# Kernel tuning notes

Measured on AMD Instinct MI355X. Metric: run time of the kernel, lower is better.

Reference implementation:

```python
import jax, jax.numpy as jnp
import numpy as np

B, S, I, H, O = 8, 2048, 1024, 4096, 1024


def setup_inputs() -> dict:
    key = jax.random.key(0)
    ks = jax.random.split(key, 7)
    s_i = 1.0 / np.sqrt(I)
    s_h = 1.0 / np.sqrt(H)
    return {
        "x": jax.random.normal(ks[0], (B, S, I), dtype=jnp.float32),
        "W1": jax.random.normal(ks[1], (H, I), dtype=jnp.float32) * s_i,
        "b1": jax.random.normal(ks[2], (H,), dtype=jnp.float32) * s_i,
        "W2": jax.random.normal(ks[3], (O, H), dtype=jnp.float32) * s_h,
        "b2": jax.random.normal(ks[4], (O,), dtype=jnp.float32) * s_h,
        "Wg": jax.random.normal(ks[5], (I, I), dtype=jnp.float32) * s_i,
        "bg": jax.random.normal(ks[6], (I,), dtype=jnp.float32) * s_i,
    }


def reference(x, W1, b1, W2, b2, Wg, bg):
    # Gate is a per-timestep linear on x_t only -> batch it over all timesteps.
    decay = jax.nn.sigmoid(jnp.einsum('bsi,ji->bsj', x, Wg) + bg)  # [B,S,I]
    immediate = x * decay
    delayed = (1.0 - decay) * x

    # Sequential buffer recurrence: buf_t = buf_{t-1} * decay_t + delayed_t
    def step(buf, td):
        d, dl = td
        buf = buf * d + dl
        return buf, buf

    buf0 = jnp.zeros((x.shape[0], x.shape[2]), dtype=x.dtype)
    _, bufs = jax.lax.scan(step, buf0, (jnp.swapaxes(decay, 0, 1), jnp.swapaxes(delayed, 0, 1)))  # [S,B,I]
    combined = immediate + jnp.swapaxes(bufs, 0, 1)  # [B,S,I]

    # MLP applied per timestep -> batch over (B,S).
    hidden = jax.nn.relu(jnp.einsum('bsi,hi->bsh', combined, W1) + b1)  # [B,S,H]
    out = jnp.einsum('bsh,oh->bso', hidden, W2) + b2  # [B,S,O]
    return out
```

## Files before the change

kernel.cpp:

```cpp
#include <hip/hip_runtime.h>
#include <hip/hip_bf16.h>
#include <type_traits>

using bf16 = __hip_bfloat16;

typedef __bf16 bf16x8 __attribute__((ext_vector_type(8)));
typedef unsigned short u16x8 __attribute__((ext_vector_type(8)));
typedef float f32x4 __attribute__((ext_vector_type(4)));

constexpr int Bdim = 8, Sdim = 2048, Idim = 1024, Hdim = 4096, Odim = 1024;
constexpr int CH = 64;
constexpr int CL = Sdim / CH;

#define EP_SIGMOID 0
#define EP_RELU    1
#define EP_BIAS    2

__device__ __forceinline__ void async16(void* lds, const void* g) {
    __builtin_amdgcn_global_load_lds(
        (const __attribute__((address_space(1))) unsigned int*)g,
        (__attribute__((address_space(3))) unsigned int*)lds,
        16, 0, 0);
}

__global__ __launch_bounds__(256) void cvt_f32_bf16(const float* __restrict__ in,
                                                    bf16* __restrict__ out, int n) {
    const int i = (blockIdx.x * 256 + threadIdx.x) * 4;
    if (i >= n) return;
    const float4 v = *(const float4*)(in + i);
    union { unsigned short us[4]; unsigned long long u64; } r;
    r.us[0] = __bfloat16_as_ushort(__float2bfloat16(v.x));
    r.us[1] = __bfloat16_as_ushort(__float2bfloat16(v.y));
    r.us[2] = __bfloat16_as_ushort(__float2bfloat16(v.z));
    r.us[3] = __bfloat16_as_ushort(__float2bfloat16(v.w));
    *(unsigned long long*)(out + i) = r.u64;
}

__device__ __forceinline__ u16x8 load8(const float* p) {
    const float4 v0 = *(const float4*)p;
    const float4 v1 = *(const float4*)(p + 4);
    u16x8 r;
    r[0] = __bfloat16_as_ushort(__float2bfloat16(v0.x));
    r[1] = __bfloat16_as_ushort(__float2bfloat16(v0.y));
    r[2] = __bfloat16_as_ushort(__float2bfloat16(v0.z));
    r[3] = __bfloat16_as_ushort(__float2bfloat16(v0.w));
    r[4] = __bfloat16_as_ushort(__float2bfloat16(v1.x));
    r[5] = __bfloat16_as_ushort(__float2bfloat16(v1.y));
    r[6] = __bfloat16_as_ushort(__float2bfloat16(v1.z));
    r[7] = __bfloat16_as_ushort(__float2bfloat16(v1.w));
    return r;
}
__device__ __forceinline__ u16x8 load8(const bf16* p) { return *(const u16x8*)p; }

__device__ __forceinline__ float toF(float v) { return v; }
__device__ __forceinline__ float toF(bf16 v)  { return __bfloat162float(v); }

__device__ __forceinline__ void ld4(const bf16* p, float f[4]) {
    const ushort4 v = *(const ushort4*)p;
    f[0] = __bfloat162float(__builtin_bit_cast(bf16, v.x));
    f[1] = __bfloat162float(__builtin_bit_cast(bf16, v.y));
    f[2] = __bfloat162float(__builtin_bit_cast(bf16, v.z));
    f[3] = __bfloat162float(__builtin_bit_cast(bf16, v.w));
}
__device__ __forceinline__ void ld4(const float* p, float f[4]) {
    const float4 v = *(const float4*)p;
    f[0] = v.x; f[1] = v.y; f[2] = v.z; f[3] = v.w;
}

template <int MODE, int N, int K, typename TA, typename TB, typename TO>
__global__ __launch_bounds__(256) void gemm_bt(const TA* __restrict__ A,
                                               const TB* __restrict__ Bm,
                                               const float* __restrict__ bias,
                                               TO* __restrict__ outp,
                                               int Mt) {
    __shared__ __align__(16) unsigned short Alds[128 * 32];
    __shared__ __align__(16) unsigned short Blds[128 * 32];

    const int tid  = threadIdx.x;
    const int lane = tid & 63;
    const int wave = tid >> 6;
    const int wr = wave >> 1, wc = wave & 1;
    const int quad = lane >> 4, l15 = lane & 15;

    constexpr int Nt = N >> 7;
    constexpr int GRP = 8;
    constexpr int gsz = GRP * Nt;
    const int g   = blockIdx.x / gsz;
    const int rem = blockIdx.x - g * gsz;
    const int mbase = g * GRP;
    int msz = Mt - mbase; if (msz > GRP) msz = GRP;
    const int m_idx = mbase + rem % msz;
    const int n_idx = rem / msz;
    const int m0 = m_idx * 128;
    const int n0 = n_idx * 128;

    const int srow = tid >> 2;
    const int scol = (tid & 3) * 8;
    const TA* ag0 = A  + (size_t)(m0 + srow) * K + scol;
    const TA* ag1 = ag0 + (size_t)64 * K;
    const TB* bg0 = Bm + (size_t)(n0 + srow) * K + scol;
    const TB* bg1 = bg0 + (size_t)64 * K;
    unsigned short* al0 = Alds + tid * 8;
    unsigned short* al1 = al0 + 2048;
    unsigned short* bl0 = Blds + tid * 8;
    unsigned short* bl1 = bl0 + 2048;

    f32x4 acc[4][4];
#pragma unroll
    for (int i = 0; i < 4; ++i)
#pragma unroll
        for (int j = 0; j < 4; ++j) acc[i][j] = {0.f, 0.f, 0.f, 0.f};

    constexpr bool FAST = std::is_same_v<TA, bf16> && std::is_same_v<TB, bf16>;

#pragma unroll 8
    for (int k0 = 0; k0 < K; k0 += 32) {
        if constexpr (FAST) {
            async16(al0, ag0); async16(al1, ag1);
            async16(bl0, bg0); async16(bl1, bg1);
        } else {
            const u16x8 a0 = load8(ag0), a1 = load8(ag1);
            const u16x8 b0 = load8(bg0), b1 = load8(bg1);
            *(u16x8*)al0 = a0; *(u16x8*)al1 = a1;
            *(u16x8*)bl0 = b0; *(u16x8*)bl1 = b1;
        }
        ag0 += 32; ag1 += 32; bg0 += 32; bg1 += 32;
        __syncthreads();

        bf16x8 af[4], bfv[4];
#pragma unroll
        for (int mi = 0; mi < 4; ++mi) {
            const u16x8 t = *(const u16x8*)(Alds + (wr * 64 + mi * 16 + l15) * 32 + quad * 8);
            af[mi] = __builtin_bit_cast(bf16x8, t);
        }
#pragma unroll
        for (int ni = 0; ni < 4; ++ni) {
            const u16x8 t = *(const u16x8*)(Blds + (wc * 64 + ni * 16 + l15) * 32 + quad * 8);
            bfv[ni] = __builtin_bit_cast(bf16x8, t);
        }
#pragma unroll
        for (int mi = 0; mi < 4; ++mi)
#pragma unroll
            for (int ni = 0; ni < 4; ++ni)
                acc[mi][ni] = __builtin_amdgcn_mfma_f32_16x16x32_bf16(af[mi], bfv[ni], acc[mi][ni], 0, 0, 0);
        __syncthreads();
    }

#pragma unroll
    for (int ni = 0; ni < 4; ++ni) {
        const int ncol = n0 + wc * 64 + ni * 16 + l15;
        const float bv = bias[ncol];
#pragma unroll
        for (int mi = 0; mi < 4; ++mi) {
            const int mrow = m0 + wr * 64 + mi * 16 + quad * 4;
#pragma unroll
            for (int r = 0; r < 4; ++r) {
                float v = acc[mi][ni][r] + bv;
                if constexpr (MODE == EP_SIGMOID) v = 1.f / (1.f + __expf(-v));
                if constexpr (MODE == EP_RELU)    v = v > 0.f ? v : 0.f;
                if constexpr (std::is_same_v<TO, bf16>)
                    outp[(size_t)(mrow + r) * N + ncol] = __float2bfloat16(v);
                else
                    outp[(size_t)(mrow + r) * N + ncol] = v;
            }
        }
    }
}

template <int MODE, int BM, int N, int K, typename TO>
__global__ __launch_bounds__(512, 2) void gemm8p(const bf16* __restrict__ A,
                                                 const bf16* __restrict__ Bm,
                                                 const float* __restrict__ bias,
                                                 TO* __restrict__ outp,
                                                 int Mt) {
    static_assert(BM == 256 || BM == 128);
    constexpr int MR   = BM / 32;
    constexpr int MR2  = MR / 2;
    constexpr int ABUF = BM * 128;
    constexpr int BBUF = 256 * 128;
    constexpr int HALF_A = ABUF / 2;
    constexpr int HALF_B = BBUF / 2;
    constexpr int LA = BM / 128;
    constexpr int NT = K / 64;
    static_assert(NT % 2 == 0 && NT >= 2);

    __shared__ __align__(16) char lds[2 * ABUF + 2 * BBUF];

    const int tid  = threadIdx.x;
    const int lane = tid & 63;
    const int wave = tid >> 6;
    const int wr = wave >> 2;
    const int wc = wave & 3;
    const int quad = lane >> 4, l15 = lane & 15;

    constexpr int Nt = N / 256;
    const int nwg = Mt * Nt;
    int b = blockIdx.x;
    if ((nwg & 7) == 0) { const int cpx = nwg >> 3; b = (b & 7) * cpx + (b >> 3); }
    const int m_idx = b % Mt;
    const int n_idx = b / Mt;
    const int m0 = m_idx * BM;
    const int n0 = n_idx * 256;

    const int loff = (l15 * 64 + quad * 16) ^ ((l15 >> 3) << 5);

    char* const Ab0 = lds;
    char* const Ab1 = lds + ABUF;
    char* const Bb0 = lds + 2 * ABUF;
    char* const Bb1 = lds + 2 * ABUF + BBUF;

    int rowS[2], klS[2];
#pragma unroll
    for (int l = 0; l < 2; ++l) {
        const int s = l * 512 + tid;
        const int c = s & 63;
        const int e = c ^ (((c >> 5) & 1) << 1);
        rowS[l] = ((s >> 7) << 4) + (e >> 2);
        klS[l]  = ((s >> 6) & 1) * 32 + (e & 3) * 8;
    }
    const bf16* pa[2]; const bf16* pb[2];
#pragma unroll
    for (int l = 0; l < 2; ++l) {
        pa[l] = A  + (size_t)(m0 + rowS[l]) * K + klS[l];
        pb[l] = Bm + (size_t)(n0 + rowS[l]) * K + klS[l];
    }

    auto stageA = [&](char* dst, int h, int kt) {
#pragma unroll
        for (int l = 0; l < LA; ++l)
            async16(dst + h * HALF_A + (l * 512 + tid) * 16,
                    pa[l] + (size_t)h * (BM / 2) * K + (size_t)kt * 64);
    };
    auto stageB = [&](char* dst, int h, int kt) {
#pragma unroll
        for (int l = 0; l < 2; ++l)
            async16(dst + h * HALF_B + (l * 512 + tid) * 16,
                    pb[l] + (size_t)h * 128 * K + (size_t)kt * 64);
    };
    auto ldA = [&](const char* abase, int mi_g, int ks) -> bf16x8 {
        return __builtin_bit_cast(bf16x8,
            *(const u16x8*)(abase + (((wr * MR + mi_g) * 2 + ks) << 10) + loff));
    };
    auto ldB = [&](const char* bbase, int ni, int ks) -> bf16x8 {
        return __builtin_bit_cast(bf16x8,
            *(const u16x8*)(bbase + (((wc * 4 + ni) * 2 + ks) << 10) + loff));
    };

    f32x4 acc[MR][4];
#pragma unroll
    for (int i = 0; i < MR; ++i)
#pragma unroll
        for (int j = 0; j < 4; ++j) acc[i][j] = {0.f, 0.f, 0.f, 0.f};
    bf16x8 a[MR2][2], bb[4][2];

    stageA(Ab0, 0, 0); stageA(Ab0, 1, 0);
    stageB(Bb0, 0, 0); stageB(Bb0, 1, 0);
    stageB(Bb1, 0, 1); stageB(Bb1, 1, 1);
    asm volatile("s_waitcnt vmcnt(4)" ::: "memory");
    __builtin_amdgcn_s_barrier();

#define FENCE() asm volatile("" ::: "memory")
#define MFMA_Q(AR, NI0)                                                         \
    _Pragma("unroll") for (int mi = 0; mi < MR2; ++mi)                          \
    _Pragma("unroll") for (int ni = 0; ni < 2; ++ni)                            \
    _Pragma("unroll") for (int ks = 0; ks < 2; ++ks)                            \
        acc[(AR) + mi][(NI0) + ni] = __builtin_amdgcn_mfma_f32_16x16x32_bf16(   \
            a[mi][ks], bb[(NI0) + ni][ks], acc[(AR) + mi][(NI0) + ni], 0, 0, 0);

#define KTILE(T, AB, BB, AN)                                                    \
    {                                                                           \
        const int t_ = (T);                                                     \
                                     \
        _Pragma("unroll") for (int mi = 0; mi < MR2; ++mi)                      \
        _Pragma("unroll") for (int ks = 0; ks < 2; ++ks)                        \
            a[mi][ks] = ldA(AB, mi, ks);                                        \
        _Pragma("unroll") for (int ni = 0; ni < 2; ++ni)                        \
        _Pragma("unroll") for (int ks = 0; ks < 2; ++ks)                        \
            bb[ni][ks] = ldB(BB, ni, ks);                                       \
        if (t_ + 1 < NT) stageA(AN, 0, t_ + 1);                                 \
        FENCE(); __builtin_amdgcn_s_barrier(); FENCE();                         \
        __builtin_amdgcn_s_setprio(1);                                          \
        MFMA_Q(0, 0)                                                            \
        __builtin_amdgcn_s_setprio(0);                                          \
                                            \
        _Pragma("unroll") for (int ni = 0; ni < 2; ++ni)                        \
        _Pragma("unroll") for (int ks = 0; ks < 2; ++ks)                        \
            bb[2 + ni][ks] = ldB(BB, 2 + ni, ks);                               \
        if (t_ + 1 < NT) stageA(AN, 1, t_ + 1);                                 \
        FENCE(); __builtin_amdgcn_s_barrier(); FENCE();                         \
        __builtin_amdgcn_s_setprio(1);                                          \
        MFMA_Q(0, 2)                                                            \
        __builtin_amdgcn_s_setprio(0);                                          \
                                                           \
        _Pragma("unroll") for (int mi = 0; mi < MR2; ++mi)                      \
        _Pragma("unroll") for (int ks = 0; ks < 2; ++ks)                        \
            a[mi][ks] = ldA(AB, MR2 + mi, ks);                                  \
        FENCE(); __builtin_amdgcn_s_barrier(); FENCE();                         \
        __builtin_amdgcn_s_setprio(1);                                          \
        MFMA_Q(MR2, 0)                                                          \
        __builtin_amdgcn_s_setprio(0);                                          \
                       \
        if (t_ + 2 < NT) { stageB(BB, 0, t_ + 2); stageB(BB, 1, t_ + 2); }      \
        if (t_ + 2 < NT) { asm volatile("s_waitcnt vmcnt(4)" ::: "memory"); }   \
        else             { asm volatile("s_waitcnt vmcnt(0)" ::: "memory"); }   \
        FENCE(); __builtin_amdgcn_s_barrier(); FENCE();                         \
        __builtin_amdgcn_s_setprio(1);                                          \
        MFMA_Q(MR2, 2)                                                          \
        __builtin_amdgcn_s_setprio(0);                                          \
    }

#pragma unroll 1
    for (int t = 0; t < NT; t += 2) {
        KTILE(t,     Ab0, Bb0, Ab1)
        KTILE(t + 1, Ab1, Bb1, Ab0)
    }
#undef KTILE
#undef MFMA_Q
#undef FENCE

    float bv[4];
#pragma unroll
    for (int ni = 0; ni < 4; ++ni) bv[ni] = bias[n0 + wc * 64 + ni * 16 + l15];
#pragma unroll
    for (int mi = 0; mi < MR; ++mi) {
        const int mrow = m0 + wr * (MR * 16) + mi * 16 + quad * 4;
#pragma unroll
        for (int r = 0; r < 4; ++r) {
            TO* rowp = outp + (size_t)(mrow + r) * N + n0 + wc * 64 + l15;
#pragma unroll
            for (int ni = 0; ni < 4; ++ni) {
                float v = acc[mi][ni][r] + bv[ni];
                if constexpr (MODE == EP_SIGMOID) v = 1.f / (1.f + __expf(-v));
                if constexpr (MODE == EP_RELU)    v = v > 0.f ? v : 0.f;
                if constexpr (std::is_same_v<TO, bf16>)
                    rowp[ni * 16] = __float2bfloat16(v);
                else
                    rowp[ni * 16] = v;
            }
        }
    }
}

template <typename XT>
__global__ __launch_bounds__(256) void scan_p1(const XT* __restrict__ x,
                                               const bf16* __restrict__ decay,
                                               float* __restrict__ P,
                                               float* __restrict__ Q) {
    const int bc = blockIdx.x;
    const int c = bc & (CH - 1);
    const int b = bc / CH;
    const int i = threadIdx.x * 4;
    size_t idx = ((size_t)(b * Sdim + c * CL)) * Idim + i;
    float p[4] = {1.f, 1.f, 1.f, 1.f};
    float q[4] = {0.f, 0.f, 0.f, 0.f};
#pragma unroll 4
    for (int j = 0; j < CL; ++j) {
        float d[4], xx[4];
        ld4(decay + idx, d);
        ld4(x + idx, xx);
#pragma unroll
        for (int k = 0; k < 4; ++k) {
            q[k] = q[k] * d[k] + (1.f - d[k]) * xx[k];
            p[k] *= d[k];
        }
        idx += Idim;
    }
    *(float4*)(P + (size_t)bc * Idim + i) = {p[0], p[1], p[2], p[3]};
    *(float4*)(Q + (size_t)bc * Idim + i) = {q[0], q[1], q[2], q[3]};
}

__global__ __launch_bounds__(256) void scan_p2(const float* __restrict__ P,
                                               const float* __restrict__ Q,
                                               float* __restrict__ buf0,
                                               int G) {
    const int g = blockIdx.x * 256 + threadIdx.x;
    const int b = g >> 10;
    const int i = g & (Idim - 1);
    if (b >= G) return;
    float buf = 0.f;
    for (int c = 0; c < CH; ++c) {
        const size_t o = ((size_t)(b * CH + c)) * Idim + i;
        buf0[o] = buf;
        buf = P[o] * buf + Q[o];
    }
}

template <typename XT>
__global__ __launch_bounds__(256) void scan_p3(const XT* __restrict__ x,
                                               const bf16* __restrict__ decay,
                                               const float* __restrict__ buf0,
                                               bf16* __restrict__ comb) {
    const int bc = blockIdx.x;
    const int c = bc & (CH - 1);
    const int b = bc / CH;
    const int i = threadIdx.x * 4;
    size_t idx = ((size_t)(b * Sdim + c * CL)) * Idim + i;
    float buf[4];
    {
        const float4 v = *(const float4*)(buf0 + (size_t)bc * Idim + i);
        buf[0] = v.x; buf[1] = v.y; buf[2] = v.z; buf[3] = v.w;
    }
#pragma unroll 4
    for (int j = 0; j < CL; ++j) {
        float d[4], xx[4];
        ld4(decay + idx, d);
        ld4(x + idx, xx);
        ushort4 o;
#pragma unroll
        for (int k = 0; k < 4; ++k)
            buf[k] = buf[k] * d[k] + (1.f - d[k]) * xx[k];
        o.x = __bfloat16_as_ushort(__float2bfloat16(xx[0] * d[0] + buf[0]));
        o.y = __bfloat16_as_ushort(__float2bfloat16(xx[1] * d[1] + buf[1]));
        o.z = __bfloat16_as_ushort(__float2bfloat16(xx[2] * d[2] + buf[2]));
        o.w = __bfloat16_as_ushort(__float2bfloat16(xx[3] * d[3] + buf[3]));
        *(ushort4*)(comb + idx) = o;
        idx += Idim;
    }
}

extern "C" void kernel_launch(void* const* d_in, const int* in_sizes, int n_in,
                              void* d_out, int out_size, void* d_ws, size_t ws_size,
                              hipStream_t stream) {
    const float* x  = (const float*)d_in[0];
    const float* W1 = (const float*)d_in[1];
    const float* b1 = (const float*)d_in[2];
    const float* W2 = (const float*)d_in[3];
    const float* b2 = (const float*)d_in[4];
    const float* Wg = (const float*)d_in[5];
    const float* bg = (const float*)d_in[6];
    float* out = (float*)d_out;

    const dim3 blk(256);
    const dim3 blk512(512);

    const size_t nW1 = (size_t)Hdim * Idim;
    const size_t nW2 = (size_t)Odim * Hdim;
    const size_t nWg = (size_t)Idim * Idim;
    const size_t wCopies = (nW1 + nW2 + nWg) * 2;

    const size_t xbB   = (size_t)Sdim * Idim * 2;
    const size_t dB    = xbB;
    const size_t cmbB  = xbB;
    const size_t pB    = (size_t)CH * Idim * 4;
    const size_t perBatch = xbB + dB + cmbB + 3 * pB;

    int G = 0;
    if (ws_size >= wCopies + 8 * perBatch) G = 8;
    else if (ws_size >= wCopies + 4 * perBatch) G = 4;
    else if (ws_size >= wCopies + 2 * perBatch) G = 2;
    else if (ws_size >= wCopies + 1 * perBatch) G = 1;

    if (G > 0) {
        char* p = (char*)d_ws;
        bf16* W1b = (bf16*)p;  p += nW1 * 2;
        bf16* W2b = (bf16*)p;  p += nW2 * 2;
        bf16* Wgb = (bf16*)p;  p += nWg * 2;
        bf16*  xb   = (bf16*)p;
        bf16*  decay= (bf16*)(p + (size_t)G * xbB);
        bf16*  comb = (bf16*)(p + (size_t)G * (xbB + dB));
        float* P    = (float*)(p + (size_t)G * (xbB + dB + cmbB));
        float* Q    = (float*)(p + (size_t)G * (xbB + dB + cmbB + pB));
        float* buf0 = (float*)(p + (size_t)G * (xbB + dB + cmbB + 2 * pB));
        bf16*  hid  = xb;
        const int chunk_rows = G * 1024;

        cvt_f32_bf16<<<(int)(nW1 / 1024), blk, 0, stream>>>(W1, W1b, (int)nW1);
        cvt_f32_bf16<<<(int)(nW2 / 1024), blk, 0, stream>>>(W2, W2b, (int)nW2);
        cvt_f32_bf16<<<(int)(nWg / 1024), blk, 0, stream>>>(Wg, Wgb, (int)nWg);

        for (int b0 = 0; b0 < Bdim; b0 += G) {
            const float* xg = x + (size_t)b0 * Sdim * Idim;
            const int rowsG = G * Sdim;
            const int nXg = rowsG * Idim;

            cvt_f32_bf16<<<nXg / 1024, blk, 0, stream>>>(xg, xb, nXg);

            gemm8p<EP_SIGMOID, 256, Idim, Idim, bf16>
                <<<(rowsG / 256) * (Idim / 256), blk512, 0, stream>>>(
                    xb, Wgb, bg, decay, rowsG / 256);

            scan_p1<bf16><<<G * CH, blk, 0, stream>>>(xb, decay, P, Q);
            scan_p2<<<G * Idim / 256, blk, 0, stream>>>(P, Q, buf0, G);
            scan_p3<bf16><<<G * CH, blk, 0, stream>>>(xb, decay, buf0, comb);

            for (int r0 = 0; r0 < rowsG; r0 += chunk_rows) {
                const int rows = (rowsG - r0 < chunk_rows) ? rowsG - r0 : chunk_rows;
                gemm8p<EP_RELU, 256, Hdim, Idim, bf16>
                    <<<(rows / 256) * (Hdim / 256), blk512, 0, stream>>>(
                        comb + (size_t)r0 * Idim, W1b, b1, hid, rows / 256);
                gemm8p<EP_BIAS, 128, Odim, Hdim, float>
                    <<<(rows / 128) * (Odim / 256), blk512, 0, stream>>>(
                        hid, W2b, b2, out + (size_t)(b0 * Sdim + r0) * Odim, rows / 128);
            }
        }
    } else {
        char* p = (char*)d_ws;
        bf16*  decay= (bf16*)p;
        bf16*  comb = (bf16*)(p + dB);
        float* P    = (float*)(p + dB + cmbB);
        float* Q    = (float*)(p + dB + cmbB + pB);
        float* buf0 = (float*)(p + dB + cmbB + 2 * pB);
        char*  hp   = p + dB + cmbB + 3 * pB;
        size_t rem  = (ws_size > (size_t)(hp - (char*)d_ws))
                        ? ws_size - (size_t)(hp - (char*)d_ws) : 0;
        int chunk_rows = (int)((rem / ((size_t)Hdim * 2)) / 128) * 128;
        if (chunk_rows < 128) chunk_rows = 128;
        if (chunk_rows > Sdim) chunk_rows = Sdim;
        bf16* hid = (bf16*)hp;

        for (int b0 = 0; b0 < Bdim; ++b0) {
            const float* xg = x + (size_t)b0 * Sdim * Idim;

            gemm_bt<EP_SIGMOID, Idim, Idim, float, float, bf16>
                <<<(Idim / 128) * (Sdim / 128), blk, 0, stream>>>(
                    xg, Wg, bg, decay, Sdim / 128);

            scan_p1<float><<<CH, blk, 0, stream>>>(xg, decay, P, Q);
            scan_p2<<<Idim / 256, blk, 0, stream>>>(P, Q, buf0, 1);
            scan_p3<float><<<CH, blk, 0, stream>>>(xg, decay, buf0, comb);

            for (int r0 = 0; r0 < Sdim; r0 += chunk_rows) {
                const int rows = (Sdim - r0 < chunk_rows) ? Sdim - r0 : chunk_rows;
                gemm_bt<EP_RELU, Hdim, Idim, bf16, float, bf16>
                    <<<(Hdim / 128) * (rows / 128), blk, 0, stream>>>(
                        comb + (size_t)r0 * Idim, W1, b1, hid, rows / 128);
                gemm_bt<EP_BIAS, Odim, Hdim, bf16, float, float>
                    <<<(Odim / 128) * (rows / 128), blk, 0, stream>>>(
                        hid, W2, b2, out + (size_t)(b0 * Sdim + r0) * Odim, rows / 128);
            }
        }
    }
}
```

Baseline: 504.3 us.

## Restructure GEMM main loop to prefetch next-tile fragments and cut barriers

Reorganizes the k-tile loop of the bf16 MFMA GEMM to use four distinct fragment register sets (aL, aH, b0f, b2f). The first A and B fragments of the next tile are loaded from LDS during the last MFMA quarter of the current tile, and barriers per tile drop from four to two. This aims to overlap LDS reads with matrix math and reduce synchronization stalls, at the cost of more VGPRs per thread. The scan chunk length CH also doubles from 64 to 128, changing the chunked recurrence granularity.

```diff
diff --git a/kernel.cpp b/kernel.cpp
--- a/kernel.cpp
+++ b/kernel.cpp
@@ -9,7 +9,7 @@
 typedef float f32x4 __attribute__((ext_vector_type(4)));
 
 constexpr int Bdim = 8, Sdim = 2048, Idim = 1024, Hdim = 4096, Odim = 1024;
-constexpr int CH = 64;
+constexpr int CH = 128;
 constexpr int CL = Sdim / CH;
 
 #define EP_SIGMOID 0
@@ -182,7 +182,7 @@
     constexpr int HALF_B = BBUF / 2;
     constexpr int LA = BM / 128;
     constexpr int NT = K / 64;
-    static_assert(NT % 2 == 0 && NT >= 2);
+    static_assert(NT % 2 == 0 && NT >= 4);
 
     __shared__ __align__(16) char lds[2 * ABUF + 2 * BBUF];
 
@@ -203,6 +203,8 @@
     const int n0 = n_idx * 256;
 
     const int loff = (l15 * 64 + quad * 16) ^ ((l15 >> 3) << 5);
+    const int aol = wr * (MR * 2048) + loff;
+    const int bol = wc * 8192 + loff;
 
     char* const Ab0 = lds;
     char* const Ab1 = lds + ABUF;
@@ -239,11 +241,11 @@
     };
     auto ldA = [&](const char* abase, int mi_g, int ks) -> bf16x8 {
         return __builtin_bit_cast(bf16x8,
-            *(const u16x8*)(abase + (((wr * MR + mi_g) * 2 + ks) << 10) + loff));
+            *(const u16x8*)(abase + aol + (((mi_g) * 2 + ks) << 10)));
     };
     auto ldB = [&](const char* bbase, int ni, int ks) -> bf16x8 {
         return __builtin_bit_cast(bf16x8,
-            *(const u16x8*)(bbase + (((wc * 4 + ni) * 2 + ks) << 10) + loff));
+            *(const u16x8*)(bbase + bol + (((ni) * 2 + ks) << 10)));
     };
 
     f32x4 acc[MR][4];
@@ -251,68 +253,67 @@
     for (int i = 0; i < MR; ++i)
 #pragma unroll
         for (int j = 0; j < 4; ++j) acc[i][j] = {0.f, 0.f, 0.f, 0.f};
-    bf16x8 a[MR2][2], bb[4][2];
+    bf16x8 aL[MR2][2], aH[MR2][2], b0f[2][2], b2f[2][2];
 
     stageA(Ab0, 0, 0); stageA(Ab0, 1, 0);
     stageB(Bb0, 0, 0); stageB(Bb0, 1, 0);
     stageB(Bb1, 0, 1); stageB(Bb1, 1, 1);
     asm volatile("s_waitcnt vmcnt(4)" ::: "memory");
     __builtin_amdgcn_s_barrier();
+    asm volatile("" ::: "memory");
+#pragma unroll
+    for (int mi = 0; mi < MR2; ++mi)
+#pragma unroll
+        for (int ks = 0; ks < 2; ++ks) aL[mi][ks] = ldA(Ab0, mi, ks);
+#pragma unroll
+    for (int ni = 0; ni < 2; ++ni)
+#pragma unroll
+        for (int ks = 0; ks < 2; ++ks) b0f[ni][ks] = ldB(Bb0, ni, ks);
 
 #define FENCE() asm volatile("" ::: "memory")
-#define MFMA_Q(AR, NI0)                                                         \
+#define MFMA_Q(AR, NI0, AF, BF)                                                 \
+    __builtin_amdgcn_s_setprio(1);                                              \
     _Pragma("unroll") for (int mi = 0; mi < MR2; ++mi)                          \
     _Pragma("unroll") for (int ni = 0; ni < 2; ++ni)                            \
     _Pragma("unroll") for (int ks = 0; ks < 2; ++ks)                            \
         acc[(AR) + mi][(NI0) + ni] = __builtin_amdgcn_mfma_f32_16x16x32_bf16(   \
-            a[mi][ks], bb[(NI0) + ni][ks], acc[(AR) + mi][(NI0) + ni], 0, 0, 0);
-
-#define KTILE(T, AB, BB, AN)                                                    \
+            AF[mi][ks], BF[ni][ks], acc[(AR) + mi][(NI0) + ni], 0, 0, 0);       \
+    __builtin_amdgcn_s_setprio(0);
+
+#define KTILE(T, AB, BB, AN, BN)                                                \
     {                                                                           \
         const int t_ = (T);                                                     \
-                                     \
+                                 \
+        _Pragma("unroll") for (int ni = 0; ni < 2; ++ni)                        \
+        _Pragma("unroll") for (int ks = 0; ks < 2; ++ks)                        \
+            b2f[ni][ks] = ldB(BB, 2 + ni, ks);                                  \
         _Pragma("unroll") for (int mi = 0; mi < MR2; ++mi)                      \
         _Pragma("unroll") for (int ks = 0; ks < 2; ++ks)                        \
-            a[mi][ks] = ldA(AB, mi, ks);                                        \
-        _Pragma("unroll") for (int ni = 0; ni < 2; ++ni)                        \
-        _Pragma("unroll") for (int ks = 0; ks < 2; ++ks)                        \
-            bb[ni][ks] = ldB(BB, ni, ks);                                       \
-        if (t_ + 1 < NT) stageA(AN, 0, t_ + 1);                                 \
-        FENCE(); __builtin_amdgcn_s_barrier(); FENCE();                         \
-        __builtin_amdgcn_s_setprio(1);                                          \
-        MFMA_Q(0, 0)                                                            \
-        __builtin_amdgcn_s_setprio(0);                                          \
-                                            \
-        _Pragma("unroll") for (int ni = 0; ni < 2; ++ni)                        \
-        _Pragma("unroll") for (int ks = 0; ks < 2; ++ks)                        \
-            bb[2 + ni][ks] = ldB(BB, 2 + ni, ks);                               \
-        if (t_ + 1 < NT) stageA(AN, 1, t_ + 1);                                 \
-        FENCE(); __builtin_amdgcn_s_barrier(); FENCE();                         \
-        __builtin_amdgcn_s_setprio(1);                                          \
-        MFMA_Q(0, 2)                                                            \
-        __builtin_amdgcn_s_setprio(0);                                          \
-                                                           \
-        _Pragma("unroll") for (int mi = 0; mi < MR2; ++mi)                      \
-        _Pragma("unroll") for (int ks = 0; ks < 2; ++ks)                        \
-            a[mi][ks] = ldA(AB, MR2 + mi, ks);                                  \
-        FENCE(); __builtin_amdgcn_s_barrier(); FENCE();                         \
-        __builtin_amdgcn_s_setprio(1);                                          \
-        MFMA_Q(MR2, 0)                                                          \
-        __builtin_amdgcn_s_setprio(0);                                          \
-                       \
+            aH[mi][ks] = ldA(AB, MR2 + mi, ks);                                 \
+        if (t_ + 1 < NT) { stageA(AN, 0, t_ + 1); stageA(AN, 1, t_ + 1); }      \
+        MFMA_Q(0, 0, aL, b0f)                 \
+        MFMA_Q(0, 2, aL, b2f)                       \
+        FENCE(); __builtin_amdgcn_s_barrier(); FENCE();            \
         if (t_ + 2 < NT) { stageB(BB, 0, t_ + 2); stageB(BB, 1, t_ + 2); }      \
+        MFMA_Q(MR2, 0, aH, b0f)                  \
         if (t_ + 2 < NT) { asm volatile("s_waitcnt vmcnt(4)" ::: "memory"); }   \
         else             { asm volatile("s_waitcnt vmcnt(0)" ::: "memory"); }   \
-        FENCE(); __builtin_amdgcn_s_barrier(); FENCE();                         \
-        __builtin_amdgcn_s_setprio(1);                                          \
-        MFMA_Q(MR2, 2)                                                          \
-        __builtin_amdgcn_s_setprio(0);                                          \
+        FENCE(); __builtin_amdgcn_s_barrier(); FENCE();            \
+        if (t_ + 1 < NT) {                                                      \
+            _Pragma("unroll") for (int mi = 0; mi < MR2; ++mi)                  \
+            _Pragma("unroll") for (int ks = 0; ks < 2; ++ks)                    \
+                aL[mi][ks] = ldA(AN, mi, ks);                                   \
+            _Pragma("unroll") for (int ni = 0; ni < 2; ++ni)                    \
+            _Pragma("unroll") for (int ks = 0; ks < 2; ++ks)                    \
+                b0f[ni][ks] = ldB(BN, ni, ks);                                  \
+        }                                                                       \
+        MFMA_Q(MR2, 2, aH, b2f)                                   \
     }
 
 #pragma unroll 1
     for (int t = 0; t < NT; t += 2) {
-        KTILE(t,     Ab0, Bb0, Ab1)
-        KTILE(t + 1, Ab1, Bb1, Ab0)
+        KTILE(t,     Ab0, Bb0, Ab1, Bb1)
+        KTILE(t + 1, Ab1, Bb1, Ab0, Bb0)
     }
 #undef KTILE
 #undef MFMA_Q
```

After: 480.4 us. 4.7% less time.

## Deepen A-tile prefetch in GEMM pipeline and double the scan chunk length

Applied to the files above, without the earlier changes.

Restructures the GEMM main loop so the first half of the A tile for k-tile t+2 is staged early into the buffer being consumed, and the second half for t+1 is issued sooner. This gives global-to-LDS loads more time in flight, and the vmcnt wait threshold is adjusted to match. B fragments are split into two register sets so the second-half MFMAs reuse already-loaded B data, and per-wave LDS offsets are precomputed. The scan chunk size CH also goes from 64 to 128, which changes how the recurrence is parallelised. Overwriting A-buffer halves early risks races if the barrier placement is not exact.

```diff
diff --git a/kernel.cpp b/kernel.cpp
--- a/kernel.cpp
+++ b/kernel.cpp
@@ -9,7 +9,7 @@
 typedef float f32x4 __attribute__((ext_vector_type(4)));
 
 constexpr int Bdim = 8, Sdim = 2048, Idim = 1024, Hdim = 4096, Odim = 1024;
-constexpr int CH = 64;
+constexpr int CH = 128;
 constexpr int CL = Sdim / CH;
 
 #define EP_SIGMOID 0
@@ -182,7 +182,8 @@
     constexpr int HALF_B = BBUF / 2;
     constexpr int LA = BM / 128;
     constexpr int NT = K / 64;
-    static_assert(NT % 2 == 0 && NT >= 2);
+    static_assert(NT % 2 == 0 && NT >= 4);
+    constexpr int VMC = LA + 4;
 
     __shared__ __align__(16) char lds[2 * ABUF + 2 * BBUF];
 
@@ -203,6 +204,8 @@
     const int n0 = n_idx * 256;
 
     const int loff = (l15 * 64 + quad * 16) ^ ((l15 >> 3) << 5);
+    const int aol = wr * (MR * 2048) + loff;
+    const int bol = wc * 8192 + loff;
 
     char* const Ab0 = lds;
     char* const Ab1 = lds + ABUF;
@@ -239,11 +242,11 @@
     };
     auto ldA = [&](const char* abase, int mi_g, int ks) -> bf16x8 {
         return __builtin_bit_cast(bf16x8,
-            *(const u16x8*)(abase + (((wr * MR + mi_g) * 2 + ks) << 10) + loff));
+            *(const u16x8*)(abase + aol + (((mi_g) * 2 + ks) << 10)));
     };
     auto ldB = [&](const char* bbase, int ni, int ks) -> bf16x8 {
         return __builtin_bit_cast(bf16x8,
-            *(const u16x8*)(bbase + (((wc * 4 + ni) * 2 + ks) << 10) + loff));
+            *(const u16x8*)(bbase + bol + (((ni) * 2 + ks) << 10)));
     };
 
     f32x4 acc[MR][4];
@@ -251,62 +254,60 @@
     for (int i = 0; i < MR; ++i)
 #pragma unroll
         for (int j = 0; j < 4; ++j) acc[i][j] = {0.f, 0.f, 0.f, 0.f};
-    bf16x8 a[MR2][2], bb[4][2];
+    bf16x8 a[MR2][2], b0f[2][2], b2f[2][2];
 
     stageA(Ab0, 0, 0); stageA(Ab0, 1, 0);
     stageB(Bb0, 0, 0); stageB(Bb0, 1, 0);
+    stageA(Ab1, 0, 1);
     stageB(Bb1, 0, 1); stageB(Bb1, 1, 1);
-    asm volatile("s_waitcnt vmcnt(4)" ::: "memory");
+    asm volatile("s_waitcnt vmcnt(%0)" :: "i"(VMC) : "memory");
     __builtin_amdgcn_s_barrier();
 
 #define FENCE() asm volatile("" ::: "memory")
-#define MFMA_Q(AR, NI0)                                                         \
+#define MFMA_Q(AR, NI0, BF)                                                     \
+    __builtin_amdgcn_s_setprio(1);                                              \
     _Pragma("unroll") for (int mi = 0; mi < MR2; ++mi)                          \
     _Pragma("unroll") for (int ni = 0; ni < 2; ++ni)                            \
     _Pragma("unroll") for (int ks = 0; ks < 2; ++ks)                            \
         acc[(AR) + mi][(NI0) + ni] = __builtin_amdgcn_mfma_f32_16x16x32_bf16(   \
-            a[mi][ks], bb[(NI0) + ni][ks], acc[(AR) + mi][(NI0) + ni], 0, 0, 0);
+            a[mi][ks], BF[ni][ks], acc[(AR) + mi][(NI0) + ni], 0, 0, 0);        \
+    __builtin_amdgcn_s_setprio(0);
 
 #define KTILE(T, AB, BB, AN)                                                    \
     {                                                                           \
         const int t_ = (T);                                                     \
-                                     \
+                                      \
         _Pragma("unroll") for (int mi = 0; mi < MR2; ++mi)                      \
         _Pragma("unroll") for (int ks = 0; ks < 2; ++ks)                        \
             a[mi][ks] = ldA(AB, mi, ks);                                        \
         _Pragma("unroll") for (int ni = 0; ni < 2; ++ni)                        \
         _Pragma("unroll") for (int ks = 0; ks < 2; ++ks)                        \
-            bb[ni][ks] = ldB(BB, ni, ks);                                       \
-        if (t_ + 1 < NT) stageA(AN, 0, t_ + 1);                                 \
+            b0f[ni][ks] = ldB(BB, ni, ks);                                      \
+        if (t_ + 1 < NT) stageA(AN, 1, t_ + 1);                                 \
         FENCE(); __builtin_amdgcn_s_barrier(); FENCE();                         \
-        __builtin_amdgcn_s_setprio(1);                                          \
-        MFMA_Q(0, 0)                                                            \
-        __builtin_amdgcn_s_setprio(0);                                          \
-                                            \
+        MFMA_Q(0, 0, b0f)                                                       \
+                                                            \
         _Pragma("unroll") for (int ni = 0; ni < 2; ++ni)                        \
         _Pragma("unroll") for (int ks = 0; ks < 2; ++ks)                        \
-            bb[2 + ni][ks] = ldB(BB, 2 + ni, ks);                               \
-        if (t_ + 1 < NT) stageA(AN, 1, t_ + 1);                                 \
+            b2f[ni][ks] = ldB(BB, 2 + ni, ks);                                  \
         FENCE(); __builtin_amdgcn_s_barrier(); FENCE();                         \
-        __builtin_amdgcn_s_setprio(1);                                          \
-        MFMA_Q(0, 2)                                                            \
-        __builtin_amdgcn_s_setprio(0);                                          \
-                                                           \
+        MFMA_Q(0, 2, b2f)                                                       \
+                \
         _Pragma("unroll") for (int mi = 0; mi < MR2; ++mi)                      \
         _Pragma("unroll") for (int ks = 0; ks < 2; ++ks)                        \
             a[mi][ks] = ldA(AB, MR2 + mi, ks);                                  \
+        if (t_ + 2 < NT) stageA(AB, 0, t_ + 2);                                 \
         FENCE(); __builtin_amdgcn_s_barrier(); FENCE();                         \
-        __builtin_amdgcn_s_setprio(1);                                          \
-        MFMA_Q(MR2, 0)                                                          \
-        __builtin_amdgcn_s_setprio(0);                                          \
-                       \
-        if (t_ + 2 < NT) { stageB(BB, 0, t_ + 2); stageB(BB, 1, t_ + 2); }      \
-        if (t_ + 2 < NT) { asm volatile("s_waitcnt vmcnt(4)" ::: "memory"); }   \
-        else             { asm volatile("s_waitcnt vmcnt(0)" ::: "memory"); }   \
+        MFMA_Q(MR2, 0, b0f)                                                     \
+                        \
+        if (t_ + 2 < NT) {                                                      \
+            stageB(BB, 0, t_ + 2); stageB(BB, 1, t_ + 2);                       \
+            asm volatile("s_waitcnt vmcnt(%0)" :: "i"(VMC) : "memory");         \
+        } else {                                                                \
+            asm volatile("s_waitcnt vmcnt(0)" ::: "memory");                    \
+        }                                                                       \
         FENCE(); __builtin_amdgcn_s_barrier(); FENCE();                         \
-        __builtin_amdgcn_s_setprio(1);                                          \
-        MFMA_Q(MR2, 2)                                                          \
-        __builtin_amdgcn_s_setprio(0);                                          \
+        MFMA_Q(MR2, 2, b2f)                                                     \
     }
 
 #pragma unroll 1
```

Result: faster. 487.5 us (-3.3%).
